# Kernel optimization log

Hardware: AMD Instinct MI355X
Metric: run time of the kernel (lower is better)

## Reference

```python
import jax, jax.numpy as jnp
import numpy as np

N, C, O, H, S, SHARE = 30000, 128, 128, 8, 16, 8
D = O // H            # mid_planes = 16
OS = O // SHARE       # 16
OFFSETS = [15000, 30000]
EPS = 1e-5


def _knn(p, offsets, k):
    """Exact per-batch KNN (incl. self), chunked to bound memory."""
    n = p.shape[0]
    idx = np.empty((n, k), dtype=np.int64)
    start = 0
    for end in offsets:
        pb = p[start:end]
        sq = (pb * pb).sum(-1)
        for qs in range(0, pb.shape[0], 1024):
            q = pb[qs:qs + 1024]
            d = sq[qs:qs + q.shape[0], None] - 2.0 * (q @ pb.T) + sq[None, :]
            part = np.argpartition(d, k - 1, axis=1)[:, :k]
            idx[start + qs:start + qs + q.shape[0]] = part + start
        start = end
    return idx


def _ln(x, g, b):
    m = x.mean(-1, keepdims=True)
    v = ((x - m) ** 2).mean(-1, keepdims=True)
    return (x - m) / jnp.sqrt(v + EPS) * g + b


def setup_inputs() -> dict:
    rng = np.random.default_rng(0)
    p_np = (rng.standard_normal((N, 3)) * 5.0).astype(np.float32)
    idx = _knn(p_np, OFFSETS, S)

    key = jax.random.key(0)
    ks = jax.random.split(key, 12)

    def lin(k, i, o):
        return (jax.random.normal(k, (i, o), jnp.float32) / np.sqrt(i)).astype(jnp.float32)

    return {
        "p": jnp.asarray(p_np),
        "x": jax.random.normal(ks[0], (N, C), jnp.float32),
        "idx": jnp.asarray(idx),
        "Wq": lin(ks[1], C, O), "bq": jnp.zeros((O,), jnp.float32),
        "Wk": lin(ks[2], C, O), "bk": jnp.zeros((O,), jnp.float32),
        "Wv": lin(ks[3], C, O), "bv": jnp.zeros((O,), jnp.float32),
        "Wp1": lin(ks[4], 3, 3), "bp1": jnp.zeros((3,), jnp.float32),
        "gp": jnp.ones((3,), jnp.float32), "betap": jnp.zeros((3,), jnp.float32),
        "Wp2": lin(ks[5], 3, O), "bp2": jnp.zeros((O,), jnp.float32),
        "gw1": jnp.ones((D,), jnp.float32), "betaw1": jnp.zeros((D,), jnp.float32),
        "Ww1": lin(ks[6], D, OS), "bw1": jnp.zeros((OS,), jnp.float32),
        "gw2": jnp.ones((OS,), jnp.float32), "betaw2": jnp.zeros((OS,), jnp.float32),
        "Ww2": lin(ks[7], OS, OS), "bw2": jnp.zeros((OS,), jnp.float32),
    }


def reference(p, x, idx, Wq, bq, Wk, bk, Wv, bv, Wp1, bp1, gp, betap, Wp2, bp2,
              gw1, betaw1, Ww1, bw1, gw2, betaw2, Ww2, bw2):
    xq = (x @ Wq + bq).reshape(N, H, D)          # (N,H,D)
    xk = x @ Wk + bk                              # (N,O)
    xv = x @ Wv + bv
    kg = xk[idx].reshape(N, S, H, D)              # neighbor gather
    vg = xv[idx].reshape(N, S, H, D)
    pr = p[idx] - p[:, None, :]                   # relative coords (N,S,3)
    pe = jax.nn.relu(_ln(pr @ Wp1 + bp1, gp, betap)) @ Wp2 + bp2  # (N,S,O)
    pe = pe.reshape(N, S, H, D)
    r = kg + pe - xq[:, None]                     # (N,S,H,D)
    w = jax.nn.relu(_ln(r, gw1, betaw1)) @ Ww1 + bw1
    w = jax.nn.relu(_ln(w, gw2, betaw2)) @ Ww2 + bw2  # (N,S,H,OS)
    w = jax.nn.softmax(w.mean(-1), axis=1)        # softmax over the S neighbors
    out = ((vg + pe) * w[..., None]).sum(axis=1)  # weighted neighbor reduce
    return out.reshape(N, O)
```

## Files before the change

kernel.cpp:

```cpp
#include <hip/hip_runtime.h>
#include <math.h>

typedef unsigned int  uint;
typedef unsigned short ushort;

constexpr int NPTS = 30000;
constexpr int CIN  = 128;
constexpr int OC   = 128;
constexpr int NH   = 8;
constexpr int NS   = 16;
constexpr int DH   = 16;
constexpr int OSH  = 16;
constexpr float EPSF = 1e-5f;

typedef __attribute__((ext_vector_type(8))) __fp16 h8;
typedef __attribute__((ext_vector_type(4))) float  f32x4;
typedef __attribute__((ext_vector_type(2))) __fp16 h2;

__device__ __forceinline__ ushort f2h(float f) {
    __fp16 h = (__fp16)f;
    return *(ushort*)&h;
}
__device__ __forceinline__ uint pk2(float a, float b) {
    h2 v = __builtin_amdgcn_cvt_pkrtz(a, b);
    return *(uint*)&v;
}
__device__ __forceinline__ h2 asH2(uint u) { return *(h2*)&u; }

#if defined(__has_builtin)
#if __has_builtin(__builtin_elementwise_max)
#define PKMAX(a, b) __builtin_elementwise_max(a, b)
#endif
#endif
#ifndef PKMAX
__device__ __forceinline__ h2 PKMAX(h2 a, h2 b) {
    h2 r; r[0] = a[0] > b[0] ? a[0] : b[0]; r[1] = a[1] > b[1] ? a[1] : b[1]; return r;
}
#endif

constexpr int PK_WW1   = 0;
constexpr int PK_WP2   = 128;
constexpr int PK_BP2   = 320;
constexpr int PK_GW1   = 384;
constexpr int PK_BW1P  = 392;
constexpr int PK_GW2   = 400;
constexpr int PK_BW2P  = 408;
constexpr int PK_RM    = 416;
constexpr int PKF_BW1  = 424;
constexpr int PKF_RMB  = 440;

__global__ __launch_bounds__(256) void prep_kernel(
    const float* __restrict__ Wq, const float* __restrict__ Wk, const float* __restrict__ Wv,
    const float* __restrict__ Wp2, const float* __restrict__ bp2,
    const float* __restrict__ gw1, const float* __restrict__ betaw1,
    const float* __restrict__ Ww1, const float* __restrict__ bw1,
    const float* __restrict__ gw2, const float* __restrict__ betaw2,
    const float* __restrict__ Ww2, const float* __restrict__ bw2,
    ushort* __restrict__ WT, uint* __restrict__ PK)
{
    const int b = blockIdx.x;
    const int t = threadIdx.x;
    if (b < 24) {
        const int mat = b >> 3;
        const int cg  = b & 7;
        const float* W = (mat == 0) ? Wq : (mat == 1 ? Wk : Wv);
        const int col = cg * 16 + (t >> 4);
        const int k0  = (t & 15) * 8;
        float v0 = W[(k0 + 0) * OC + col], v1 = W[(k0 + 1) * OC + col];
        float v2 = W[(k0 + 2) * OC + col], v3 = W[(k0 + 3) * OC + col];
        float v4 = W[(k0 + 4) * OC + col], v5 = W[(k0 + 5) * OC + col];
        float v6 = W[(k0 + 6) * OC + col], v7 = W[(k0 + 7) * OC + col];
        uint4 u = make_uint4(pk2(v0, v1), pk2(v2, v3), pk2(v4, v5), pk2(v6, v7));
        *(uint4*)&WT[(size_t)mat * OC * CIN + (size_t)col * CIN + k0] = u;
    } else {
        float* FPK = (float*)PK;
        if (t < 128) {
            int dp = t >> 4, o = t & 15;
            PK[PK_WW1 + t] = pk2(Ww1[(2 * dp) * OSH + o], Ww1[(2 * dp + 1) * OSH + o]);
        }
        if (t < 192) {
            int c = t >> 6, jj = t & 63;
            PK[PK_WP2 + t] = pk2(Wp2[c * OC + 2 * jj], Wp2[c * OC + 2 * jj + 1]);
        }
        if (t < 64)
            PK[PK_BP2 + t] = pk2(bp2[2 * t], bp2[2 * t + 1]);
        if (t < 8) {
            PK[PK_GW1 + t]  = pk2(gw1[2 * t],    gw1[2 * t + 1]);
            PK[PK_BW1P + t] = pk2(betaw1[2 * t], betaw1[2 * t + 1]);
            PK[PK_GW2 + t]  = pk2(gw2[2 * t],    gw2[2 * t + 1]);
            PK[PK_BW2P + t] = pk2(betaw2[2 * t], betaw2[2 * t + 1]);
            float r0 = 0.f, r1 = 0.f;
            #pragma unroll
            for (int o2 = 0; o2 < OSH; ++o2) {
                r0 += Ww2[(2 * t) * OSH + o2];
                r1 += Ww2[(2 * t + 1) * OSH + o2];
            }
            PK[PK_RM + t] = pk2(r0 * (1.f / OSH), r1 * (1.f / OSH));
        }
        if (t < 16)
            FPK[PKF_BW1 + t] = bw1[t];
        if (t == 16) {
            float acc = 0.f;
            #pragma unroll
            for (int o2 = 0; o2 < OSH; ++o2) acc += bw2[o2];
            FPK[PKF_RMB] = acc * (1.f / OSH);
        }
    }
}

__global__ __launch_bounds__(256) void qkv_mfma(
    const float* __restrict__ x, const ushort* __restrict__ WT,
    const float* __restrict__ bq, const float* __restrict__ bk, const float* __restrict__ bv,
    ushort* __restrict__ yq, ushort* __restrict__ yk, ushort* __restrict__ yv)
{
    const int mat = blockIdx.y;
    const float* bias = (mat == 0) ? bq : (mat == 1 ? bk : bv);
    ushort* y         = (mat == 0) ? yq : (mat == 1 ? yk : yv);
    const ushort* T   = WT + (size_t)mat * OC * CIN;

    const int n0   = blockIdx.x * 128;
    const int t    = threadIdx.x;
    const int wave = t >> 6;
    const int lane = t & 63;
    const int m16  = lane & 15;
    const int quad = lane >> 4;

    f32x4 acc[2][8];
    #pragma unroll
    for (int mt = 0; mt < 2; ++mt)
        #pragma unroll
        for (int nt = 0; nt < 8; ++nt)
            acc[mt][nt] = (f32x4){0.f, 0.f, 0.f, 0.f};

    int r0i = n0 + wave * 32 + m16;
    int r1i = r0i + 16;
    if (r0i > NPTS - 1) r0i = NPTS - 1;
    if (r1i > NPTS - 1) r1i = NPTS - 1;
    const float* arow0 = x + (size_t)r0i * CIN;
    const float* arow1 = x + (size_t)r1i * CIN;

    #pragma unroll
    for (int ks = 0; ks < 4; ++ks) {
        const int kb = ks * 32 + quad * 8;
        float4 f00 = *(const float4*)(arow0 + kb);
        float4 f01 = *(const float4*)(arow0 + kb + 4);
        float4 f10 = *(const float4*)(arow1 + kb);
        float4 f11 = *(const float4*)(arow1 + kb + 4);
        uint4 ua0 = make_uint4(pk2(f00.x, f00.y), pk2(f00.z, f00.w),
                               pk2(f01.x, f01.y), pk2(f01.z, f01.w));
        uint4 ua1 = make_uint4(pk2(f10.x, f10.y), pk2(f10.z, f10.w),
                               pk2(f11.x, f11.y), pk2(f11.z, f11.w));
        h8 a0 = *(h8*)&ua0;
        h8 a1 = *(h8*)&ua1;
        #pragma unroll
        for (int nt = 0; nt < 8; ++nt) {
            h8 bfr = *(const h8*)(T + (size_t)(nt * 16 + m16) * CIN + kb);
            acc[0][nt] = __builtin_amdgcn_mfma_f32_16x16x32_f16(a0, bfr, acc[0][nt], 0, 0, 0);
            acc[1][nt] = __builtin_amdgcn_mfma_f32_16x16x32_f16(a1, bfr, acc[1][nt], 0, 0, 0);
        }
    }

    #pragma unroll
    for (int mt = 0; mt < 2; ++mt) {
        #pragma unroll
        for (int nt = 0; nt < 8; ++nt) {
            const int col = nt * 16 + m16;
            const float bcol = bias[col];
            #pragma unroll
            for (int r = 0; r < 4; ++r) {
                int row = n0 + wave * 32 + mt * 16 + quad * 4 + r;
                if (row < NPTS)
                    y[(size_t)row * OC + col] = f2h(acc[mt][nt][r] + bcol);
            }
        }
    }
}

__global__ __launch_bounds__(128) void attn_kernel(
    const float* __restrict__ p, const int* __restrict__ idx,
    const ushort* __restrict__ xq, const ushort* __restrict__ xk, const ushort* __restrict__ xv,
    const float* __restrict__ Wp1, const float* __restrict__ bp1,
    const float* __restrict__ gp,  const float* __restrict__ betap,
    const uint* __restrict__ PK,
    float* __restrict__ out)
{
    const int n = blockIdx.x;
    const int t = threadIdx.x;
    const int s = t & 15;
    const int h = t >> 4;

    const float* FPK = (const float*)PK;

    __shared__ uint s_c[NS][68];

    const int j = idx[n * NS + s];

    float t0, t1, t2;
    {
        float pr0 = p[j * 3 + 0] - p[n * 3 + 0];
        float pr1 = p[j * 3 + 1] - p[n * 3 + 1];
        float pr2 = p[j * 3 + 2] - p[n * 3 + 2];
        float u[3];
        #pragma unroll
        for (int c = 0; c < 3; ++c)
            u[c] = bp1[c] + pr0 * Wp1[0 * 3 + c] + pr1 * Wp1[1 * 3 + c] + pr2 * Wp1[2 * 3 + c];
        float m   = (u[0] + u[1] + u[2]) * (1.f / 3.f);
        float d0 = u[0] - m, d1 = u[1] - m, d2 = u[2] - m;
        float var = (d0 * d0 + d1 * d1 + d2 * d2) * (1.f / 3.f);
        float inv = rsqrtf(var + EPSF);
        t0 = fmaxf((u[0] - m) * inv * gp[0] + betap[0], 0.f);
        t1 = fmaxf((u[1] - m) * inv * gp[1] + betap[1], 0.f);
        t2 = fmaxf((u[2] - m) * inv * gp[2] + betap[2], 0.f);
    }

    const int obase = h * DH;

    __attribute__((aligned(16))) h2 pe2[8];
    {
        h2 t02 = asH2(pk2(t0, t0));
        h2 t12 = asH2(pk2(t1, t1));
        h2 t22 = asH2(pk2(t2, t2));
        const uint* W0p = PK + PK_WP2 + 0 * 64 + h * 8;
        const uint* W1p = PK + PK_WP2 + 1 * 64 + h * 8;
        const uint* W2p = PK + PK_WP2 + 2 * 64 + h * 8;
        const uint* Bp  = PK + PK_BP2 + h * 8;
        #pragma unroll
        for (int i = 0; i < 8; ++i) {
            h2 acc = asH2(Bp[i]);
            acc = acc + t02 * asH2(W0p[i]);
            acc = acc + t12 * asH2(W1p[i]);
            acc = acc + t22 * asH2(W2p[i]);
            pe2[i] = acc;
        }
    }

    __attribute__((aligned(16))) h2 v2[8], r2[8];
    {
        __attribute__((aligned(16))) h2 k2[8], q2[8];
        const uint4* k4 = (const uint4*)(xk + (size_t)j * OC + obase);
        const uint4* v4 = (const uint4*)(xv + (size_t)j * OC + obase);
        const uint4* q4 = (const uint4*)(xq + (size_t)n * OC + obase);
        *(uint4*)&k2[0] = k4[0]; *(uint4*)&k2[4] = k4[1];
        *(uint4*)&v2[0] = v4[0]; *(uint4*)&v2[4] = v4[1];
        *(uint4*)&q2[0] = q4[0]; *(uint4*)&q2[4] = q4[1];
        #pragma unroll
        for (int i = 0; i < 8; ++i)
            r2[i] = (k2[i] + pe2[i]) - q2[i];
    }

    __attribute__((aligned(16))) h2 a2[8];
    {
        h2 sum2 = r2[0];
        #pragma unroll
        for (int i = 1; i < 8; ++i) sum2 = sum2 + r2[i];
        float m = ((float)sum2[0] + (float)sum2[1]) * (1.f / DH);
        h2 m2 = asH2(pk2(m, m));
        h2 vs2 = {(__fp16)0.f, (__fp16)0.f};
        #pragma unroll
        for (int i = 0; i < 8; ++i) {
            r2[i] = r2[i] - m2;
            vs2 = vs2 + r2[i] * r2[i];
        }
        float var = ((float)vs2[0] + (float)vs2[1]) * (1.f / DH);
        float inv = rsqrtf(var + EPSF);
        h2 inv2 = asH2(pk2(inv, inv));
        h2 z2 = {(__fp16)0.f, (__fp16)0.f};
        #pragma unroll
        for (int i = 0; i < 8; ++i) {
            h2 gi = asH2(PK[PK_GW1 + i]) * inv2;
            a2[i] = PKMAX(r2[i] * gi + asH2(PK[PK_BW1P + i]), z2);
        }
    }

    float w1[OSH];
    #pragma unroll
    for (int o2 = 0; o2 < OSH; ++o2) w1[o2] = FPK[PKF_BW1 + o2];
    #pragma unroll
    for (int dp = 0; dp < 8; ++dp) {
        #pragma unroll
        for (int o2 = 0; o2 < OSH; ++o2)
            w1[o2] = __builtin_amdgcn_fdot2(a2[dp], asH2(PK[PK_WW1 + dp * 16 + o2]), w1[o2], false);
    }

    float logit;
    {
        __attribute__((aligned(16))) h2 w2[8];
        #pragma unroll
        for (int i = 0; i < 8; ++i) w2[i] = asH2(pk2(w1[2 * i], w1[2 * i + 1]));
        h2 sum2 = w2[0];
        #pragma unroll
        for (int i = 1; i < 8; ++i) sum2 = sum2 + w2[i];
        float m = ((float)sum2[0] + (float)sum2[1]) * (1.f / OSH);
        h2 m2 = asH2(pk2(m, m));
        h2 vs2 = {(__fp16)0.f, (__fp16)0.f};
        #pragma unroll
        for (int i = 0; i < 8; ++i) {
            w2[i] = w2[i] - m2;
            vs2 = vs2 + w2[i] * w2[i];
        }
        float var = ((float)vs2[0] + (float)vs2[1]) * (1.f / OSH);
        float inv = rsqrtf(var + EPSF);
        h2 inv2 = asH2(pk2(inv, inv));
        h2 z2 = {(__fp16)0.f, (__fp16)0.f};
        logit = FPK[PKF_RMB];
        #pragma unroll
        for (int i = 0; i < 8; ++i) {
            h2 gi = asH2(PK[PK_GW2 + i]) * inv2;
            h2 bv2 = PKMAX(w2[i] * gi + asH2(PK[PK_BW2P + i]), z2);
            logit = __builtin_amdgcn_fdot2(bv2, asH2(PK[PK_RM + i]), logit, false);
        }
    }

    float w;
    {
        float mx = logit;
        #pragma unroll
        for (int mask = 1; mask < 16; mask <<= 1)
            mx = fmaxf(mx, __shfl_xor(mx, mask));
        float e = __expf(logit - mx);
        float den = e;
        #pragma unroll
        for (int mask = 1; mask < 16; mask <<= 1)
            den += __shfl_xor(den, mask);
        w = e * __builtin_amdgcn_rcpf(den);
    }

    {
        h2 w2p = asH2(pk2(w, w));
        __attribute__((aligned(16))) h2 c2[8];
        #pragma unroll
        for (int i = 0; i < 8; ++i)
            c2[i] = (v2[i] + pe2[i]) * w2p;
        *(uint4*)&s_c[s][h * 8]     = *(uint4*)&c2[0];
        *(uint4*)&s_c[s][h * 8 + 4] = *(uint4*)&c2[4];
    }
    __syncthreads();

    {
        const int oh = t >> 4;
        const int od = t & 15;
        const int col = oh * 8 + (od >> 1);
        h2 acc2 = {(__fp16)0.f, (__fp16)0.f};
        #pragma unroll
        for (int ss = 0; ss < NS; ++ss)
            acc2 = acc2 + asH2(s_c[ss][col]);
        out[(size_t)n * OC + t] = (float)acc2[od & 1];
    }
}

extern "C" void kernel_launch(void* const* d_in, const int* in_sizes, int n_in,
                              void* d_out, int out_size, void* d_ws, size_t ws_size,
                              hipStream_t stream) {
    const float* p     = (const float*)d_in[0];
    const float* x     = (const float*)d_in[1];
    const int*   idx   = (const int*)d_in[2];
    const float* Wq    = (const float*)d_in[3];
    const float* bq    = (const float*)d_in[4];
    const float* Wk    = (const float*)d_in[5];
    const float* bk    = (const float*)d_in[6];
    const float* Wv    = (const float*)d_in[7];
    const float* bv    = (const float*)d_in[8];
    const float* Wp1   = (const float*)d_in[9];
    const float* bp1   = (const float*)d_in[10];
    const float* gp    = (const float*)d_in[11];
    const float* betap = (const float*)d_in[12];
    const float* Wp2   = (const float*)d_in[13];
    const float* bp2   = (const float*)d_in[14];
    const float* gw1   = (const float*)d_in[15];
    const float* betaw1= (const float*)d_in[16];
    const float* Ww1   = (const float*)d_in[17];
    const float* bw1   = (const float*)d_in[18];
    const float* gw2   = (const float*)d_in[19];
    const float* betaw2= (const float*)d_in[20];
    const float* Ww2   = (const float*)d_in[21];
    const float* bw2   = (const float*)d_in[22];
    float* out = (float*)d_out;

    ushort* WT = (ushort*)d_ws;
    ushort* xq = WT + 3 * OC * CIN;
    ushort* xk = xq + (size_t)NPTS * OC;
    ushort* xv = xk + (size_t)NPTS * OC;
    uint*   PACKS = (uint*)(xv + (size_t)NPTS * OC);

    prep_kernel<<<25, 256, 0, stream>>>(Wq, Wk, Wv,
                                        Wp2, bp2, gw1, betaw1,
                                        Ww1, bw1, gw2, betaw2, Ww2, bw2,
                                        WT, PACKS);

    dim3 g1((NPTS + 127) / 128, 3);
    qkv_mfma<<<g1, 256, 0, stream>>>(x, WT, bq, bk, bv, xq, xk, xv);

    attn_kernel<<<NPTS, 128, 0, stream>>>(p, idx, xq, xk, xv,
                                          Wp1, bp1, gp, betap,
                                          PACKS, out);
}
```

Before: 190.1 us.

## Compute per-neighbor Ww1 projection with MFMA via LDS transpose

Replaces the per-thread 16x8 fdot2 loop for the first weight-encoding linear layer with four MFMA 16x16x32 f16 ops per wave. Activations are staged through shared memory so they can be loaded in MFMA fragment layout, and results are written back to shared memory to return to a row-per-thread layout. The Ww1 fragment is built from global weights in every block. This trades VALU dot products for matrix-core work plus extra LDS round trips and an added barrier.

New measurement: 192.7 us. No clear change (+1.4%).

```diff
diff --git a/kernel.cpp b/kernel.cpp
--- a/kernel.cpp
+++ b/kernel.cpp
@@ -181,6 +181,7 @@
     const ushort* __restrict__ xq, const ushort* __restrict__ xk, const ushort* __restrict__ xv,
     const float* __restrict__ Wp1, const float* __restrict__ bp1,
     const float* __restrict__ gp,  const float* __restrict__ betap,
+    const float* __restrict__ Ww1,
     const uint* __restrict__ PK,
     float* __restrict__ out)
 {
@@ -188,10 +189,28 @@
     const int t = threadIdx.x;
     const int s = t & 15;
     const int h = t >> 4;
+    const int lane = t & 63;
+    const int wv   = t >> 6;
 
     const float* FPK = (const float*)PK;
 
-    __shared__ uint s_c[NS][68];
+    __shared__ __attribute__((aligned(16))) char pool[2 * 64 * 80];
+    char* aw = pool + wv * (64 * 80);
+
+    h8 bfrag;
+    {
+        uint4 u = make_uint4(0u, 0u, 0u, 0u);
+        const int c = lane & 15;
+        const int q = lane >> 4;
+        if (q < 2) {
+            const float* wp = Ww1 + (q * 8) * OSH + c;
+            u.x = pk2(wp[0 * OSH], wp[1 * OSH]);
+            u.y = pk2(wp[2 * OSH], wp[3 * OSH]);
+            u.z = pk2(wp[4 * OSH], wp[5 * OSH]);
+            u.w = pk2(wp[6 * OSH], wp[7 * OSH]);
+        }
+        bfrag = *(h8*)&u;
+    }
 
     const int j = idx[n * NS + s];
 
@@ -234,9 +253,9 @@
         }
     }
 
-    __attribute__((aligned(16))) h2 v2[8], r2[8];
-    {
-        __attribute__((aligned(16))) h2 k2[8], q2[8];
+    __attribute__((aligned(16))) h2 vp2[8], r2[8];
+    {
+        __attribute__((aligned(16))) h2 k2[8], q2[8], v2[8];
         const uint4* k4 = (const uint4*)(xk + (size_t)j * OC + obase);
         const uint4* v4 = (const uint4*)(xv + (size_t)j * OC + obase);
         const uint4* q4 = (const uint4*)(xq + (size_t)n * OC + obase);
@@ -244,8 +263,10 @@
         *(uint4*)&v2[0] = v4[0]; *(uint4*)&v2[4] = v4[1];
         *(uint4*)&q2[0] = q4[0]; *(uint4*)&q2[4] = q4[1];
         #pragma unroll
-        for (int i = 0; i < 8; ++i)
-            r2[i] = (k2[i] + pe2[i]) - q2[i];
+        for (int i = 0; i < 8; ++i) {
+            r2[i]  = (k2[i] + pe2[i]) - q2[i];
+            vp2[i] = v2[i] + pe2[i];
+        }
     }
 
     __attribute__((aligned(16))) h2 a2[8];
@@ -272,21 +293,43 @@
         }
     }
 
-    float w1[OSH];
-    #pragma unroll
-    for (int o2 = 0; o2 < OSH; ++o2) w1[o2] = FPK[PKF_BW1 + o2];
-    #pragma unroll
-    for (int dp = 0; dp < 8; ++dp) {
-        #pragma unroll
-        for (int o2 = 0; o2 < OSH; ++o2)
-            w1[o2] = __builtin_amdgcn_fdot2(a2[dp], asH2(PK[PK_WW1 + dp * 16 + o2]), w1[o2], false);
+    float w1v[16];
+    {
+        *(uint4*)(aw + lane * 80 +  0) = *(uint4*)&a2[0];
+        *(uint4*)(aw + lane * 80 + 16) = *(uint4*)&a2[4];
+
+        const int c = lane & 15;
+        const int q = lane >> 4;
+        h8 af0 = *(h8*)(aw + (0 * 16 + c) * 80 + (q & 1) * 16);
+        h8 af1 = *(h8*)(aw + (1 * 16 + c) * 80 + (q & 1) * 16);
+        h8 af2 = *(h8*)(aw + (2 * 16 + c) * 80 + (q & 1) * 16);
+        h8 af3 = *(h8*)(aw + (3 * 16 + c) * 80 + (q & 1) * 16);
+
+        const float bw1c = FPK[PKF_BW1 + c];
+        f32x4 acc0 = (f32x4){bw1c, bw1c, bw1c, bw1c};
+        f32x4 acc1 = acc0, acc2m = acc0, acc3 = acc0;
+        acc0  = __builtin_amdgcn_mfma_f32_16x16x32_f16(af0, bfrag, acc0,  0, 0, 0);
+        acc1  = __builtin_amdgcn_mfma_f32_16x16x32_f16(af1, bfrag, acc1,  0, 0, 0);
+        acc2m = __builtin_amdgcn_mfma_f32_16x16x32_f16(af2, bfrag, acc2m, 0, 0, 0);
+        acc3  = __builtin_amdgcn_mfma_f32_16x16x32_f16(af3, bfrag, acc3,  0, 0, 0);
+
+        #pragma unroll
+        for (int r = 0; r < 4; ++r) {
+            *(float*)(aw + (0 * 16 + q * 4 + r) * 80 + c * 4) = acc0[r];
+            *(float*)(aw + (1 * 16 + q * 4 + r) * 80 + c * 4) = acc1[r];
+            *(float*)(aw + (2 * 16 + q * 4 + r) * 80 + c * 4) = acc2m[r];
+            *(float*)(aw + (3 * 16 + q * 4 + r) * 80 + c * 4) = acc3[r];
+        }
+        #pragma unroll
+        for (int i = 0; i < 4; ++i)
+            *(f32x4*)&w1v[4 * i] = *(const f32x4*)(aw + lane * 80 + 16 * i);
     }
 
     float logit;
     {
         __attribute__((aligned(16))) h2 w2[8];
         #pragma unroll
-        for (int i = 0; i < 8; ++i) w2[i] = asH2(pk2(w1[2 * i], w1[2 * i + 1]));
+        for (int i = 0; i < 8; ++i) w2[i] = asH2(pk2(w1v[2 * i], w1v[2 * i + 1]));
         h2 sum2 = w2[0];
         #pragma unroll
         for (int i = 1; i < 8; ++i) sum2 = sum2 + w2[i];
@@ -325,14 +368,16 @@
         w = e * __builtin_amdgcn_rcpf(den);
     }
 
+    __syncthreads();
+
     {
         h2 w2p = asH2(pk2(w, w));
         __attribute__((aligned(16))) h2 c2[8];
         #pragma unroll
         for (int i = 0; i < 8; ++i)
-            c2[i] = (v2[i] + pe2[i]) * w2p;
-        *(uint4*)&s_c[s][h * 8]     = *(uint4*)&c2[0];
-        *(uint4*)&s_c[s][h * 8 + 4] = *(uint4*)&c2[4];
+            c2[i] = vp2[i] * w2p;
+        *(uint4*)(pool + s * 272 + h * 32)      = *(uint4*)&c2[0];
+        *(uint4*)(pool + s * 272 + h * 32 + 16) = *(uint4*)&c2[4];
     }
     __syncthreads();
 
@@ -343,7 +388,7 @@
         h2 acc2 = {(__fp16)0.f, (__fp16)0.f};
         #pragma unroll
         for (int ss = 0; ss < NS; ++ss)
-            acc2 = acc2 + asH2(s_c[ss][col]);
+            acc2 = acc2 + *(const h2*)(pool + ss * 272 + col * 4);
         out[(size_t)n * OC + t] = (float)acc2[od & 1];
     }
 }
@@ -391,6 +436,6 @@
     qkv_mfma<<<g1, 256, 0, stream>>>(x, WT, bq, bk, bv, xq, xk, xv);
 
     attn_kernel<<<NPTS, 128, 0, stream>>>(p, idx, xq, xk, xv,
-                                          Wp1, bp1, gp, betap,
+                                          Wp1, bp1, gp, betap, Ww1,
                                           PACKS, out);
 }
```

## Process one point per wave with two heads per lane in attn kernel

Applied to the files above, without the earlier changes.

Restructures the attention kernel so each 64-lane wave handles one point, with four points per 256-thread block. Each lane now covers two heads (32 channels) for one neighbor. The per-point reduction goes through a private LDS slice synchronized by a wave barrier instead of a block-wide __syncthreads, and outputs are stored as float2. This removes block-level syncs and halves the lanes doing the per-neighbor positional-encoding and LayerNorm setup, at the cost of more registers per lane and serialized work for the two heads.

Result: no change. 190.6 us (+0.3%).

```diff
diff --git a/kernel.cpp b/kernel.cpp
--- a/kernel.cpp
+++ b/kernel.cpp
@@ -176,7 +176,7 @@
     }
 }
 
-__global__ __launch_bounds__(128) void attn_kernel(
+__global__ __launch_bounds__(256) void attn_kernel(
     const float* __restrict__ p, const int* __restrict__ idx,
     const ushort* __restrict__ xq, const ushort* __restrict__ xk, const ushort* __restrict__ xv,
     const float* __restrict__ Wp1, const float* __restrict__ bp1,
@@ -184,14 +184,17 @@
     const uint* __restrict__ PK,
     float* __restrict__ out)
 {
-    const int n = blockIdx.x;
-    const int t = threadIdx.x;
-    const int s = t & 15;
-    const int h = t >> 4;
+    const int t    = threadIdx.x;
+    const int wv   = t >> 6;
+    const int lane = t & 63;
+    const int n    = blockIdx.x * 4 + wv;
+    const int s    = lane & 15;
+    const int u    = lane >> 4;
 
     const float* FPK = (const float*)PK;
 
-    __shared__ uint s_c[NS][68];
+    __shared__ __attribute__((aligned(16))) char pool[4 * 16 * 272];
+    char* red = pool + wv * (16 * 272);
 
     const int j = idx[n * NS + s];
 
@@ -200,32 +203,30 @@
         float pr0 = p[j * 3 + 0] - p[n * 3 + 0];
         float pr1 = p[j * 3 + 1] - p[n * 3 + 1];
         float pr2 = p[j * 3 + 2] - p[n * 3 + 2];
-        float u[3];
+        float uu[3];
         #pragma unroll
         for (int c = 0; c < 3; ++c)
-            u[c] = bp1[c] + pr0 * Wp1[0 * 3 + c] + pr1 * Wp1[1 * 3 + c] + pr2 * Wp1[2 * 3 + c];
-        float m   = (u[0] + u[1] + u[2]) * (1.f / 3.f);
-        float d0 = u[0] - m, d1 = u[1] - m, d2 = u[2] - m;
+            uu[c] = bp1[c] + pr0 * Wp1[0 * 3 + c] + pr1 * Wp1[1 * 3 + c] + pr2 * Wp1[2 * 3 + c];
+        float m   = (uu[0] + uu[1] + uu[2]) * (1.f / 3.f);
+        float d0 = uu[0] - m, d1 = uu[1] - m, d2 = uu[2] - m;
         float var = (d0 * d0 + d1 * d1 + d2 * d2) * (1.f / 3.f);
         float inv = rsqrtf(var + EPSF);
-        t0 = fmaxf((u[0] - m) * inv * gp[0] + betap[0], 0.f);
-        t1 = fmaxf((u[1] - m) * inv * gp[1] + betap[1], 0.f);
-        t2 = fmaxf((u[2] - m) * inv * gp[2] + betap[2], 0.f);
-    }
-
-    const int obase = h * DH;
-
-    __attribute__((aligned(16))) h2 pe2[8];
+        t0 = fmaxf((uu[0] - m) * inv * gp[0] + betap[0], 0.f);
+        t1 = fmaxf((uu[1] - m) * inv * gp[1] + betap[1], 0.f);
+        t2 = fmaxf((uu[2] - m) * inv * gp[2] + betap[2], 0.f);
+    }
+
+    __attribute__((aligned(16))) h2 pe2[16];
     {
         h2 t02 = asH2(pk2(t0, t0));
         h2 t12 = asH2(pk2(t1, t1));
         h2 t22 = asH2(pk2(t2, t2));
-        const uint* W0p = PK + PK_WP2 + 0 * 64 + h * 8;
-        const uint* W1p = PK + PK_WP2 + 1 * 64 + h * 8;
-        const uint* W2p = PK + PK_WP2 + 2 * 64 + h * 8;
-        const uint* Bp  = PK + PK_BP2 + h * 8;
-        #pragma unroll
-        for (int i = 0; i < 8; ++i) {
+        const uint* W0p = PK + PK_WP2 + 0 * 64 + u * 16;
+        const uint* W1p = PK + PK_WP2 + 1 * 64 + u * 16;
+        const uint* W2p = PK + PK_WP2 + 2 * 64 + u * 16;
+        const uint* Bp  = PK + PK_BP2 + u * 16;
+        #pragma unroll
+        for (int i = 0; i < 16; ++i) {
             h2 acc = asH2(Bp[i]);
             acc = acc + t02 * asH2(W0p[i]);
             acc = acc + t12 * asH2(W1p[i]);
@@ -234,117 +235,130 @@
         }
     }
 
-    __attribute__((aligned(16))) h2 v2[8], r2[8];
+    __attribute__((aligned(16))) h2 vp2[16], r2[16];
     {
-        __attribute__((aligned(16))) h2 k2[8], q2[8];
-        const uint4* k4 = (const uint4*)(xk + (size_t)j * OC + obase);
-        const uint4* v4 = (const uint4*)(xv + (size_t)j * OC + obase);
-        const uint4* q4 = (const uint4*)(xq + (size_t)n * OC + obase);
-        *(uint4*)&k2[0] = k4[0]; *(uint4*)&k2[4] = k4[1];
-        *(uint4*)&v2[0] = v4[0]; *(uint4*)&v2[4] = v4[1];
-        *(uint4*)&q2[0] = q4[0]; *(uint4*)&q2[4] = q4[1];
-        #pragma unroll
-        for (int i = 0; i < 8; ++i)
-            r2[i] = (k2[i] + pe2[i]) - q2[i];
-    }
-
-    __attribute__((aligned(16))) h2 a2[8];
+        __attribute__((aligned(16))) h2 k2[16], q2[16], v2[16];
+        const uint4* k4 = (const uint4*)(xk + (size_t)j * OC + u * 32);
+        const uint4* v4 = (const uint4*)(xv + (size_t)j * OC + u * 32);
+        const uint4* q4 = (const uint4*)(xq + (size_t)n * OC + u * 32);
+        #pragma unroll
+        for (int i = 0; i < 4; ++i) {
+            *(uint4*)&k2[4 * i] = k4[i];
+            *(uint4*)&v2[4 * i] = v4[i];
+            *(uint4*)&q2[4 * i] = q4[i];
+        }
+        #pragma unroll
+        for (int i = 0; i < 16; ++i) {
+            r2[i]  = (k2[i] + pe2[i]) - q2[i];
+            vp2[i] = v2[i] + pe2[i];
+        }
+    }
+
+    float wgt[2];
+    #pragma unroll
+    for (int hh = 0; hh < 2; ++hh) {
+        h2* rr = r2 + hh * 8;
+
+        __attribute__((aligned(16))) h2 a2[8];
+        {
+            h2 sum2 = rr[0];
+            #pragma unroll
+            for (int i = 1; i < 8; ++i) sum2 = sum2 + rr[i];
+            float m = ((float)sum2[0] + (float)sum2[1]) * (1.f / DH);
+            h2 m2 = asH2(pk2(m, m));
+            h2 vs2 = {(__fp16)0.f, (__fp16)0.f};
+            #pragma unroll
+            for (int i = 0; i < 8; ++i) {
+                rr[i] = rr[i] - m2;
+                vs2 = vs2 + rr[i] * rr[i];
+            }
+            float var = ((float)vs2[0] + (float)vs2[1]) * (1.f / DH);
+            float inv = rsqrtf(var + EPSF);
+            h2 inv2 = asH2(pk2(inv, inv));
+            h2 z2 = {(__fp16)0.f, (__fp16)0.f};
+            #pragma unroll
+            for (int i = 0; i < 8; ++i) {
+                h2 gi = asH2(PK[PK_GW1 + i]) * inv2;
+                a2[i] = PKMAX(rr[i] * gi + asH2(PK[PK_BW1P + i]), z2);
+            }
+        }
+
+        float w1[OSH];
+        #pragma unroll
+        for (int o2 = 0; o2 < OSH; ++o2) w1[o2] = FPK[PKF_BW1 + o2];
+        #pragma unroll
+        for (int dp = 0; dp < 8; ++dp) {
+            #pragma unroll
+            for (int o2 = 0; o2 < OSH; ++o2)
+                w1[o2] = __builtin_amdgcn_fdot2(a2[dp], asH2(PK[PK_WW1 + dp * 16 + o2]), w1[o2], false);
+        }
+
+        float logit;
+        {
+            __attribute__((aligned(16))) h2 w2[8];
+            #pragma unroll
+            for (int i = 0; i < 8; ++i) w2[i] = asH2(pk2(w1[2 * i], w1[2 * i + 1]));
+            h2 sum2 = w2[0];
+            #pragma unroll
+            for (int i = 1; i < 8; ++i) sum2 = sum2 + w2[i];
+            float m = ((float)sum2[0] + (float)sum2[1]) * (1.f / OSH);
+            h2 m2 = asH2(pk2(m, m));
+            h2 vs2 = {(__fp16)0.f, (__fp16)0.f};
+            #pragma unroll
+            for (int i = 0; i < 8; ++i) {
+                w2[i] = w2[i] - m2;
+                vs2 = vs2 + w2[i] * w2[i];
+            }
+            float var = ((float)vs2[0] + (float)vs2[1]) * (1.f / OSH);
+            float inv = rsqrtf(var + EPSF);
+            h2 inv2 = asH2(pk2(inv, inv));
+            h2 z2 = {(__fp16)0.f, (__fp16)0.f};
+            logit = FPK[PKF_RMB];
+            #pragma unroll
+            for (int i = 0; i < 8; ++i) {
+                h2 gi = asH2(PK[PK_GW2 + i]) * inv2;
+                h2 bv2 = PKMAX(w2[i] * gi + asH2(PK[PK_BW2P + i]), z2);
+                logit = __builtin_amdgcn_fdot2(bv2, asH2(PK[PK_RM + i]), logit, false);
+            }
+        }
+
+        {
+            float mx = logit;
+            #pragma unroll
+            for (int mask = 1; mask < 16; mask <<= 1)
+                mx = fmaxf(mx, __shfl_xor(mx, mask));
+            float e = __expf(logit - mx);
+            float den = e;
+            #pragma unroll
+            for (int mask = 1; mask < 16; mask <<= 1)
+                den += __shfl_xor(den, mask);
+            wgt[hh] = e * __builtin_amdgcn_rcpf(den);
+        }
+    }
+
     {
-        h2 sum2 = r2[0];
-        #pragma unroll
-        for (int i = 1; i < 8; ++i) sum2 = sum2 + r2[i];
-        float m = ((float)sum2[0] + (float)sum2[1]) * (1.f / DH);
-        h2 m2 = asH2(pk2(m, m));
-        h2 vs2 = {(__fp16)0.f, (__fp16)0.f};
-        #pragma unroll
-        for (int i = 0; i < 8; ++i) {
-            r2[i] = r2[i] - m2;
-            vs2 = vs2 + r2[i] * r2[i];
-        }
-        float var = ((float)vs2[0] + (float)vs2[1]) * (1.f / DH);
-        float inv = rsqrtf(var + EPSF);
-        h2 inv2 = asH2(pk2(inv, inv));
-        h2 z2 = {(__fp16)0.f, (__fp16)0.f};
-        #pragma unroll
-        for (int i = 0; i < 8; ++i) {
-            h2 gi = asH2(PK[PK_GW1 + i]) * inv2;
-            a2[i] = PKMAX(r2[i] * gi + asH2(PK[PK_BW1P + i]), z2);
-        }
-    }
-
-    float w1[OSH];
-    #pragma unroll
-    for (int o2 = 0; o2 < OSH; ++o2) w1[o2] = FPK[PKF_BW1 + o2];
-    #pragma unroll
-    for (int dp = 0; dp < 8; ++dp) {
-        #pragma unroll
-        for (int o2 = 0; o2 < OSH; ++o2)
-            w1[o2] = __builtin_amdgcn_fdot2(a2[dp], asH2(PK[PK_WW1 + dp * 16 + o2]), w1[o2], false);
-    }
-
-    float logit;
+        h2 w0p = asH2(pk2(wgt[0], wgt[0]));
+        h2 w1p = asH2(pk2(wgt[1], wgt[1]));
+        __attribute__((aligned(16))) h2 c2[16];
+        #pragma unroll
+        for (int i = 0; i < 16; ++i)
+            c2[i] = vp2[i] * (i < 8 ? w0p : w1p);
+        char* wr = red + s * 272 + u * 64;
+        *(uint4*)(wr +  0) = *(uint4*)&c2[0];
+        *(uint4*)(wr + 16) = *(uint4*)&c2[4];
+        *(uint4*)(wr + 32) = *(uint4*)&c2[8];
+        *(uint4*)(wr + 48) = *(uint4*)&c2[12];
+    }
+
+    __builtin_amdgcn_wave_barrier();
+
     {
-        __attribute__((aligned(16))) h2 w2[8];
-        #pragma unroll
-        for (int i = 0; i < 8; ++i) w2[i] = asH2(pk2(w1[2 * i], w1[2 * i + 1]));
-        h2 sum2 = w2[0];
-        #pragma unroll
-        for (int i = 1; i < 8; ++i) sum2 = sum2 + w2[i];
-        float m = ((float)sum2[0] + (float)sum2[1]) * (1.f / OSH);
-        h2 m2 = asH2(pk2(m, m));
-        h2 vs2 = {(__fp16)0.f, (__fp16)0.f};
-        #pragma unroll
-        for (int i = 0; i < 8; ++i) {
-            w2[i] = w2[i] - m2;
-            vs2 = vs2 + w2[i] * w2[i];
-        }
-        float var = ((float)vs2[0] + (float)vs2[1]) * (1.f / OSH);
-        float inv = rsqrtf(var + EPSF);
-        h2 inv2 = asH2(pk2(inv, inv));
-        h2 z2 = {(__fp16)0.f, (__fp16)0.f};
-        logit = FPK[PKF_RMB];
-        #pragma unroll
-        for (int i = 0; i < 8; ++i) {
-            h2 gi = asH2(PK[PK_GW2 + i]) * inv2;
-            h2 bv2 = PKMAX(w2[i] * gi + asH2(PK[PK_BW2P + i]), z2);
-            logit = __builtin_amdgcn_fdot2(bv2, asH2(PK[PK_RM + i]), logit, false);
-        }
-    }
-
-    float w;
-    {
-        float mx = logit;
-        #pragma unroll
-        for (int mask = 1; mask < 16; mask <<= 1)
-            mx = fmaxf(mx, __shfl_xor(mx, mask));
-        float e = __expf(logit - mx);
-        float den = e;
-        #pragma unroll
-        for (int mask = 1; mask < 16; mask <<= 1)
-            den += __shfl_xor(den, mask);
-        w = e * __builtin_amdgcn_rcpf(den);
-    }
-
-    {
-        h2 w2p = asH2(pk2(w, w));
-        __attribute__((aligned(16))) h2 c2[8];
-        #pragma unroll
-        for (int i = 0; i < 8; ++i)
-            c2[i] = (v2[i] + pe2[i]) * w2p;
-        *(uint4*)&s_c[s][h * 8]     = *(uint4*)&c2[0];
-        *(uint4*)&s_c[s][h * 8 + 4] = *(uint4*)&c2[4];
-    }
-    __syncthreads();
-
-    {
-        const int oh = t >> 4;
-        const int od = t & 15;
-        const int col = oh * 8 + (od >> 1);
         h2 acc2 = {(__fp16)0.f, (__fp16)0.f};
         #pragma unroll
         for (int ss = 0; ss < NS; ++ss)
-            acc2 = acc2 + asH2(s_c[ss][col]);
-        out[(size_t)n * OC + t] = (float)acc2[od & 1];
+            acc2 = acc2 + *(const h2*)(red + ss * 272 + lane * 4);
+        float2 o2 = make_float2((float)acc2[0], (float)acc2[1]);
+        *(float2*)(out + (size_t)n * OC + lane * 2) = o2;
     }
 }
 
@@ -390,7 +404,7 @@
     dim3 g1((NPTS + 127) / 128, 3);
     qkv_mfma<<<g1, 256, 0, stream>>>(x, WT, bq, bk, bv, xq, xk, xv);
 
-    attn_kernel<<<NPTS, 128, 0, stream>>>(p, idx, xq, xk, xv,
-                                          Wp1, bp1, gp, betap,
-                                          PACKS, out);
-}
+    attn_kernel<<<NPTS / 4, 256, 0, stream>>>(p, idx, xq, xk, xv,
+                                              Wp1, bp1, gp, betap,
+                                              PACKS, out);
+}
```
